# Kernel optimization log

Measured on AMD Instinct MI355X. Metric: run time of the kernel, lower is better.

Reference implementation:

```python
import jax, jax.numpy as jnp
import numpy as np

HIDDEN = 2048
N_HEADS = 32
HEAD_DIM = HIDDEN // N_HEADS
CONV_K = 4
INTER = 5632  # 256*ceil(2048*4*2/3/256)
EPS = 1e-6


def _rms(x, w):
    return x * jax.lax.rsqrt(jnp.mean(x * x, axis=-1, keepdims=True) + EPS) * w


def _l2norm(x):
    n = jnp.sqrt(jnp.sum(x * x, axis=-1, keepdims=True))
    return x / jnp.maximum(n, 1e-12)


def _causal_dwconv(x, w):
    # x [B,T,C], w [C,K] depthwise causal conv (left pad K-1), matches conv1d(pad=K-1)[..., :T]
    C, K = w.shape
    xt = jnp.transpose(x, (0, 2, 1))  # [B,C,T]
    out = jax.lax.conv_general_dilated(
        xt, w[:, None, :], window_strides=(1,), padding=[(K - 1, 0)],
        feature_group_count=C, dimension_numbers=('NCH', 'OIH', 'NCH'))
    return jnp.transpose(out, (0, 2, 1))


def _delta_scan(k, q, v, beta):
    # k,q,v: [B,T,nh,hd]; beta: [B,T,nh]. Per-head state S [hd(v), hd(k)].
    B, T, nh, hd = k.shape
    km, qm, vm = (jnp.moveaxis(a, 1, 0) for a in (k, q, v))  # [T,B,nh,hd]
    bm = jnp.moveaxis(beta, 1, 0)  # [T,B,nh]

    def step(S, inp):
        kt, qt, vt, bt = inp
        err = jnp.einsum('bhvk,bhk->bhv', S, kt) - vt
        S = S - bt[..., None, None] * err[..., None] * kt[..., None, :]
        o = jnp.einsum('bhvk,bhk->bhv', S, qt)
        return S, o

    S0 = jnp.zeros((B, nh, hd, hd), k.dtype)
    S, o = jax.lax.scan(step, S0, (km, qm, vm, bm))
    return jnp.moveaxis(o, 0, 1), S


def setup_inputs() -> dict:
    key = jax.random.key(0)
    ks = jax.random.split(key, 12)
    s = 0.02
    d = {
        'hidden_states': jax.random.normal(ks[0], (1, 1024, HIDDEN), jnp.float32),
        'attn_norm_w': jnp.ones((HIDDEN,), jnp.float32),
        'Wq': jax.random.normal(ks[1], (HIDDEN, HIDDEN), jnp.float32) * s,
        'Wk': jax.random.normal(ks[2], (HIDDEN, HIDDEN), jnp.float32) * s,
        'Wv': jax.random.normal(ks[3], (HIDDEN, HIDDEN), jnp.float32) * s,
        'conv_q': jax.random.normal(ks[4], (HIDDEN, CONV_K), jnp.float32) * 0.1,
        'conv_k': jax.random.normal(ks[5], (HIDDEN, CONV_K), jnp.float32) * 0.1,
        'conv_v': jax.random.normal(ks[6], (HIDDEN, CONV_K), jnp.float32) * 0.1,
        'Wbeta': jax.random.normal(ks[7], (N_HEADS, HIDDEN), jnp.float32) * s,
        'out_norm_w': jnp.ones((HIDDEN,), jnp.float32),
        'Wout': jax.random.normal(ks[8], (HIDDEN, HIDDEN), jnp.float32) * s,
        'mlp_norm_w': jnp.ones((HIDDEN,), jnp.float32),
        'Wgate': jax.random.normal(ks[9], (INTER, HIDDEN), jnp.float32) * s,
        'Wup': jax.random.normal(ks[10], (INTER, HIDDEN), jnp.float32) * s,
        'Wdown': jax.random.normal(ks[11], (HIDDEN, INTER), jnp.float32) * s,
    }
    return d


def reference(hidden_states, attn_norm_w, Wq, Wk, Wv, conv_q, conv_k, conv_v,
              Wbeta, out_norm_w, Wout, mlp_norm_w, Wgate, Wup, Wdown):
    x = hidden_states
    B, T, H = x.shape
    nh, hd = N_HEADS, HEAD_DIM
    silu = jax.nn.silu

    # --- DeltaNet attention sub-block ---
    h = _rms(x, attn_norm_w)
    # proj -> causal depthwise conv -> SiLU (in conv helper) -> SiLU again (forward)
    q = silu(silu(_causal_dwconv(h @ Wq.T, conv_q)))
    k = silu(silu(_causal_dwconv(h @ Wk.T, conv_k)))
    v = silu(silu(_causal_dwconv(h @ Wv.T, conv_v)))
    q = _l2norm(q.reshape(B, T, nh, hd))
    k = _l2norm(k.reshape(B, T, nh, hd))
    v = v.reshape(B, T, nh, hd)
    beta = jax.nn.sigmoid(h @ Wbeta.T)  # [B,T,nh]

    o, memory_state = _delta_scan(k, q, v, beta)
    o = o.reshape(B, T, H)
    o = _rms(o, out_norm_w) @ Wout.T
    x = x + o

    # --- SwiGLU MLP sub-block ---
    h2 = _rms(x, mlp_norm_w)
    gate = h2 @ Wgate.T
    up = h2 @ Wup.T
    x = x + (silu(gate) * up) @ Wdown.T
    return x, memory_state
```

## Files before the change

kernel.cpp:

```cpp
#include <hip/hip_runtime.h>
#include <stdint.h>

typedef unsigned short u16;
typedef unsigned int u32;

#define T_SEQ 1024
#define HID   2048
#define NH    32
#define HD    64
#define NCHUNK 16
#define INTER 5632

typedef __attribute__((ext_vector_type(8))) short b16x8;
typedef __attribute__((ext_vector_type(4))) float f32x4;

__device__ inline float bf2f(u16 u) { union { u32 i; float f; } v; v.i = ((u32)u) << 16; return v.f; }
__device__ inline u16 f2bf(float f) {
  union { float f; u32 i; } v; v.f = f;
  u32 u = v.i;
  return (u16)((u + 0x7FFFu + ((u >> 16) & 1u)) >> 16);
}
__device__ inline float silu_f(float x) { return x / (1.f + __expf(-x)); }

typedef __attribute__((address_space(1))) const unsigned int as1_u32;
typedef __attribute__((address_space(3))) unsigned int as3_u32;
__device__ inline void gl_lds16(const void* g, void* l) {
  __builtin_amdgcn_global_load_lds((as1_u32*)g, (as3_u32*)l, 16, 0, 0);
}

__global__ __launch_bounds__(256) void k_cvt(const float* __restrict__ s, u16* __restrict__ d, int n4) {
  int i = blockIdx.x * 256 + threadIdx.x;
  if (i < n4) {
    float4 v = ((const float4*)s)[i];
    u32 lo = (u32)f2bf(v.x) | ((u32)f2bf(v.y) << 16);
    u32 hi = (u32)f2bf(v.z) | ((u32)f2bf(v.w) << 16);
    ((uint2*)d)[i] = make_uint2(lo, hi);
  }
}

__global__ __launch_bounds__(256) void k_rms(const float* __restrict__ x, const float* __restrict__ w,
                                             u16* __restrict__ out) {
  int row = blockIdx.x, tid = threadIdx.x;
  const float* xr = x + (size_t)row * HID;
  float4 v0 = ((const float4*)xr)[tid];
  float4 v1 = ((const float4*)xr)[tid + 256];
  float ss = v0.x * v0.x + v0.y * v0.y + v0.z * v0.z + v0.w * v0.w +
             v1.x * v1.x + v1.y * v1.y + v1.z * v1.z + v1.w * v1.w;
  for (int m = 32; m; m >>= 1) ss += __shfl_xor(ss, m, 64);
  __shared__ float wsum[4];
  if ((tid & 63) == 0) wsum[tid >> 6] = ss;
  __syncthreads();
  float tot = wsum[0] + wsum[1] + wsum[2] + wsum[3];
  float sc = rsqrtf(tot / (float)HID + 1e-6f);
  float4 w0 = ((const float4*)w)[tid];
  float4 w1 = ((const float4*)w)[tid + 256];
  u32 lo, hi;
  lo = (u32)f2bf(v0.x * sc * w0.x) | ((u32)f2bf(v0.y * sc * w0.y) << 16);
  hi = (u32)f2bf(v0.z * sc * w0.z) | ((u32)f2bf(v0.w * sc * w0.w) << 16);
  ((uint2*)out)[(size_t)row * 512 + tid] = make_uint2(lo, hi);
  lo = (u32)f2bf(v1.x * sc * w1.x) | ((u32)f2bf(v1.y * sc * w1.y) << 16);
  hi = (u32)f2bf(v1.z * sc * w1.z) | ((u32)f2bf(v1.w * sc * w1.w) << 16);
  ((uint2*)out)[(size_t)row * 512 + tid + 256] = make_uint2(lo, hi);
}

__global__ __launch_bounds__(256) void k_gemm(
    const u16* __restrict__ A,
    const u16* __restrict__ B0, const u16* __restrict__ B1, const u16* __restrict__ B2,
    float* __restrict__ C0, float* __restrict__ C1, float* __restrict__ C2,
    const float* __restrict__ resid, int M, int N, int K) {
  const u16* Bp = (blockIdx.z == 0) ? B0 : (blockIdx.z == 1 ? B1 : B2);
  float* Cp = (blockIdx.z == 0) ? C0 : (blockIdx.z == 1 ? C1 : C2);
  __shared__ __align__(16) u16 As[128 * 32];
  __shared__ __align__(16) u16 Bs[128 * 32];
  int tid = threadIdx.x;
  int m0 = blockIdx.y * 128, n0 = blockIdx.x * 128;
  int lane = tid & 63, wv = tid >> 6, wr = wv >> 1, wc = wv & 1;
  int lrow = lane & 15, quad = lane >> 4;
  int lr = lane >> 2, lc = (lane & 3) * 8;
  f32x4 acc[4][4];
#pragma unroll
  for (int i = 0; i < 4; ++i)
#pragma unroll
    for (int j = 0; j < 4; ++j) acc[i][j] = (f32x4){0.f, 0.f, 0.f, 0.f};

  for (int k0 = 0; k0 < K; k0 += 32) {
    const u16* Ag = A + (size_t)(m0 + wv * 32) * K + k0;
    const u16* Bg = Bp + (size_t)(n0 + wv * 32) * K + k0;
    gl_lds16(Ag + (size_t)lr * K + lc,        &As[(wv * 32) * 32]);
    gl_lds16(Ag + (size_t)(16 + lr) * K + lc, &As[(wv * 32 + 16) * 32]);
    gl_lds16(Bg + (size_t)lr * K + lc,        &Bs[(wv * 32) * 32]);
    gl_lds16(Bg + (size_t)(16 + lr) * K + lc, &Bs[(wv * 32 + 16) * 32]);
    __syncthreads();
    b16x8 af[4], bfr[4];
#pragma unroll
    for (int i = 0; i < 4; ++i) af[i] = *(const b16x8*)&As[(wr * 64 + i * 16 + lrow) * 32 + quad * 8];
#pragma unroll
    for (int j = 0; j < 4; ++j) bfr[j] = *(const b16x8*)&Bs[(wc * 64 + j * 16 + lrow) * 32 + quad * 8];
#pragma unroll
    for (int i = 0; i < 4; ++i)
#pragma unroll
      for (int j = 0; j < 4; ++j)
        acc[i][j] = __builtin_amdgcn_mfma_f32_16x16x32_bf16(af[i], bfr[j], acc[i][j], 0, 0, 0);
    __syncthreads();
  }
#pragma unroll
  for (int i = 0; i < 4; ++i)
#pragma unroll
    for (int j = 0; j < 4; ++j)
#pragma unroll
      for (int r = 0; r < 4; ++r) {
        int row = m0 + wr * 64 + i * 16 + quad * 4 + r;
        int col = n0 + wc * 64 + j * 16 + lrow;
        float val = acc[i][j][r];
        if (resid) val += resid[(size_t)row * N + col];
        Cp[(size_t)row * N + col] = val;
      }
}

__global__ __launch_bounds__(256) void k_beta(const u16* __restrict__ hbf, const float* __restrict__ Wb,
                                              float* __restrict__ beta) {
  __shared__ __align__(16) float hr[HID];
  __shared__ float red[256];
  int t = blockIdx.x, tid = threadIdx.x;
#pragma unroll
  for (int i = 0; i < 8; ++i) {
    int c = i * 256 + tid;
    hr[c] = bf2f(hbf[(size_t)t * HID + c]);
  }
  __syncthreads();
  int head = tid >> 3, j = tid & 7;
  const float* wrow = Wb + (size_t)head * HID + j * 256;
  const float* hs = hr + j * 256;
  float acc = 0.f;
#pragma unroll 16
  for (int c = 0; c < 256; c += 4) {
    float4 wv = *(const float4*)&wrow[c];
    float4 hv = *(const float4*)&hs[c];
    acc += hv.x * wv.x + hv.y * wv.y + hv.z * wv.z + hv.w * wv.w;
  }
  red[tid] = acc;
  __syncthreads();
  if (tid < 32) {
    float s = 0.f;
#pragma unroll
    for (int i = 0; i < 8; ++i) s += red[tid * 8 + i];
    beta[(size_t)t * NH + tid] = 1.f / (1.f + __expf(-s));
  }
}

__global__ __launch_bounds__(256) void k_conv(const float* __restrict__ proj,
                                              const float* __restrict__ cw0, const float* __restrict__ cw1,
                                              const float* __restrict__ cw2, float* __restrict__ outp) {
  int z = blockIdx.z;
  const float* src = proj + (size_t)z * T_SEQ * HID;
  float* dst = outp + (size_t)z * T_SEQ * HID;
  const float* cw = (z == 0) ? cw0 : (z == 1 ? cw1 : cw2);
  bool l2 = (z < 2);
  int c = threadIdx.x & 63, wr = threadIdx.x >> 6;
  int head = blockIdx.y;
  int ch = head * 64 + c;
  int t0 = blockIdx.x * 64 + wr * 16;
  float4 w = ((const float4*)cw)[ch];
  float xm3 = (t0 >= 3) ? src[(size_t)(t0 - 3) * HID + ch] : 0.f;
  float xm2 = (t0 >= 2) ? src[(size_t)(t0 - 2) * HID + ch] : 0.f;
  float xm1 = (t0 >= 1) ? src[(size_t)(t0 - 1) * HID + ch] : 0.f;
  for (int i = 0; i < 16; ++i) {
    int t = t0 + i;
    float x0 = src[(size_t)t * HID + ch];
    float zv = xm3 * w.x + xm2 * w.y + xm1 * w.z + x0 * w.w;
    float s = silu_f(silu_f(zv));
    if (l2) {
      float ss = s * s;
      for (int m = 32; m; m >>= 1) ss += __shfl_xor(ss, m, 64);
      float n = sqrtf(ss);
      s = s / fmaxf(n, 1e-12f);
    }
    dst[(size_t)t * HID + ch] = s;
    xm3 = xm2; xm2 = xm1; xm1 = x0;
  }
}

__global__ __launch_bounds__(256) void k_phaseA(
    const float* __restrict__ qp, const float* __restrict__ kp, const float* __restrict__ vp,
    const float* __restrict__ beta,
    u16* __restrict__ negWbf, u16* __restrict__ Uvbf, u16* __restrict__ Ktbf,
    u16* __restrict__ Qbf, u16* __restrict__ Pbf) {
  int cx = blockIdx.x, h = blockIdx.y;
  __shared__ __align__(16) u16 Kst[64 * 72];
  __shared__ __align__(16) u16 Qst[64 * 72];
  __shared__ __align__(16) float Af[64 * 68];
  __shared__ float bet[64];
  int tid = threadIdx.x;
  int t0 = cx * 64;
#pragma unroll
  for (int i = 0; i < 16; ++i) {
    int idx = i * 256 + tid, s = idx >> 6, d = idx & 63;
    size_t g = (size_t)(t0 + s) * HID + h * 64 + d;
    Kst[s * 72 + d] = f2bf(kp[g]);
    Qst[s * 72 + d] = f2bf(qp[g]);
  }
  if (tid < 64) bet[tid] = beta[(size_t)(t0 + tid) * NH + h];
  __syncthreads();
  int lane = tid & 63, wv = tid >> 6, lrow = lane & 15, quad = lane >> 4;
  f32x4 accA[4], accP[4];
#pragma unroll
  for (int i = 0; i < 4; ++i) { accA[i] = (f32x4){0.f, 0.f, 0.f, 0.f}; accP[i] = (f32x4){0.f, 0.f, 0.f, 0.f}; }
#pragma unroll
  for (int ks = 0; ks < 2; ++ks) {
    b16x8 bk = *(const b16x8*)&Kst[(wv * 16 + lrow) * 72 + ks * 32 + quad * 8];
#pragma unroll
    for (int i = 0; i < 4; ++i) {
      b16x8 ak = *(const b16x8*)&Kst[(i * 16 + lrow) * 72 + ks * 32 + quad * 8];
      b16x8 aq = *(const b16x8*)&Qst[(i * 16 + lrow) * 72 + ks * 32 + quad * 8];
      accA[i] = __builtin_amdgcn_mfma_f32_16x16x32_bf16(ak, bk, accA[i], 0, 0, 0);
      accP[i] = __builtin_amdgcn_mfma_f32_16x16x32_bf16(aq, bk, accP[i], 0, 0, 0);
    }
  }
  size_t cb2 = ((size_t)h * NCHUNK + cx) * 4096;
#pragma unroll
  for (int i = 0; i < 4; ++i)
#pragma unroll
    for (int r = 0; r < 4; ++r) {
      int srow = i * 16 + quad * 4 + r, col = wv * 16 + lrow;
      Af[srow * 68 + col] = (col < srow) ? accA[i][r] * bet[srow] : 0.f;
      Pbf[cb2 + srow * 64 + col] = f2bf((col <= srow) ? accP[i][r] : 0.f);
    }
  __syncthreads();
  if (wv < 2) {
    int c = lane;
    float x[64];
    if (wv == 0) {
#pragma unroll
      for (int s = 0; s < 64; ++s) x[s] = bet[s] * bf2f(Kst[s * 72 + c]);
    } else {
#pragma unroll
      for (int s = 0; s < 64; ++s) x[s] = bet[s] * vp[(size_t)(t0 + s) * HID + h * 64 + c];
    }
#pragma unroll
    for (int s = 1; s < 64; ++s) {
      float a = 0.f;
#pragma unroll
      for (int r = 0; r < (s & ~3); r += 4) {
        float4 av = *(const float4*)&Af[s * 68 + r];
        a += av.x * x[r] + av.y * x[r + 1] + av.z * x[r + 2] + av.w * x[r + 3];
      }
#pragma unroll
      for (int r = (s & ~3); r < s; ++r) a += Af[s * 68 + r] * x[r];
      x[s] -= a;
    }
    if (wv == 0) {
#pragma unroll
      for (int s = 0; s < 64; ++s) negWbf[cb2 + s * 64 + c] = f2bf(-x[s]);
    } else {
#pragma unroll
      for (int s = 0; s < 64; ++s) Uvbf[cb2 + s * 64 + c] = f2bf(x[s]);
    }
  } else if (wv == 2) {
#pragma unroll
    for (int it = 0; it < 8; ++it) {
      int cidx = it * 64 + lane, s = cidx >> 3, d0 = (cidx & 7) * 8;
      *(uint4*)&Qbf[cb2 + s * 64 + d0] = *(const uint4*)&Qst[s * 72 + d0];
    }
  } else {
#pragma unroll
    for (int it = 0; it < 8; ++it) {
      int cidx = it * 64 + lane, d = cidx >> 3, s0 = (cidx & 7) * 8;
      u16 tmp[8];
#pragma unroll
      for (int j = 0; j < 8; ++j) tmp[j] = Kst[(s0 + j) * 72 + d];
      *(uint4*)&Ktbf[cb2 + d * 64 + s0] = *(const uint4*)tmp;
    }
  }
}

__global__ __launch_bounds__(256) void k_phaseB1(
    const u16* __restrict__ negWbf, const u16* __restrict__ Uvbf, const u16* __restrict__ Ktbf,
    u16* __restrict__ Utws, u16* __restrict__ Sws, float* __restrict__ Sout) {
  int h = blockIdx.x, tid = threadIdx.x;
  __shared__ __align__(16) u16 S0b[2][64 * 72];
  __shared__ __align__(16) u16 Ut[64 * 72];
  int lane = tid & 63, wv = tid >> 6, lrow = lane & 15, quad = lane >> 4;
#pragma unroll
  for (int i = 0; i < 16; ++i) {
    int idx = i * 256 + tid;
    S0b[0][(idx >> 6) * 72 + (idx & 63)] = 0;
  }
  f32x4 aS[4];
#pragma unroll
  for (int i = 0; i < 4; ++i) aS[i] = (f32x4){0.f, 0.f, 0.f, 0.f};

  b16x8 Wf[2][4][2]; b16x8 Ktf[2][2]; u16 Uvr[2][4][4];
  size_t hb = (size_t)h * NCHUNK * 4096;
  {
    size_t cb2 = hb;
#pragma unroll
    for (int i = 0; i < 4; ++i)
#pragma unroll
      for (int ks = 0; ks < 2; ++ks)
        Wf[0][i][ks] = *(const b16x8*)&negWbf[cb2 + (i * 16 + lrow) * 64 + ks * 32 + quad * 8];
#pragma unroll
    for (int ks = 0; ks < 2; ++ks)
      Ktf[0][ks] = *(const b16x8*)&Ktbf[cb2 + (wv * 16 + lrow) * 64 + ks * 32 + quad * 8];
#pragma unroll
    for (int i = 0; i < 4; ++i)
#pragma unroll
      for (int r = 0; r < 4; ++r)
        Uvr[0][i][r] = Uvbf[cb2 + (i * 16 + quad * 4 + r) * 64 + wv * 16 + lrow];
  }
  __syncthreads();
#pragma unroll
  for (int cx = 0; cx < NCHUNK; ++cx) {
    const int p = cx & 1, q = p ^ 1;
    size_t cb2 = hb + (size_t)cx * 4096;
    if (cx > 0) {
#pragma unroll
      for (int i = 0; i < 2; ++i) {
        int cidx = i * 256 + tid, dv = cidx >> 3, s0 = (cidx & 7) * 8;
        *(uint4*)&Sws[cb2 + dv * 64 + s0] = *(const uint4*)&S0b[p][dv * 72 + s0];
      }
    }
    if (cx + 1 < NCHUNK) {
      size_t cbn = cb2 + 4096;
#pragma unroll
      for (int i = 0; i < 4; ++i)
#pragma unroll
        for (int ks = 0; ks < 2; ++ks)
          Wf[q][i][ks] = *(const b16x8*)&negWbf[cbn + (i * 16 + lrow) * 64 + ks * 32 + quad * 8];
#pragma unroll
      for (int ks = 0; ks < 2; ++ks)
        Ktf[q][ks] = *(const b16x8*)&Ktbf[cbn + (wv * 16 + lrow) * 64 + ks * 32 + quad * 8];
#pragma unroll
      for (int i = 0; i < 4; ++i)
#pragma unroll
        for (int r = 0; r < 4; ++r)
          Uvr[q][i][r] = Uvbf[cbn + (i * 16 + quad * 4 + r) * 64 + wv * 16 + lrow];
    }
    f32x4 aU[4];
#pragma unroll
    for (int i = 0; i < 4; ++i)
#pragma unroll
      for (int r = 0; r < 4; ++r) aU[i][r] = bf2f(Uvr[p][i][r]);
#pragma unroll
    for (int ks = 0; ks < 2; ++ks) {
      b16x8 bS = *(const b16x8*)&S0b[p][(wv * 16 + lrow) * 72 + ks * 32 + quad * 8];
#pragma unroll
      for (int i = 0; i < 4; ++i)
        aU[i] = __builtin_amdgcn_mfma_f32_16x16x32_bf16(Wf[p][i][ks], bS, aU[i], 0, 0, 0);
    }
#pragma unroll
    for (int i = 0; i < 4; ++i)
#pragma unroll
      for (int r = 0; r < 4; ++r) {
        int s = i * 16 + quad * 4 + r, dv = wv * 16 + lrow;
        Ut[dv * 72 + s] = f2bf(aU[i][r]);
      }
    __syncthreads();
#pragma unroll
    for (int i = 0; i < 2; ++i) {
      int cidx = i * 256 + tid, dv = cidx >> 3, s0 = (cidx & 7) * 8;
      *(uint4*)&Utws[cb2 + dv * 64 + s0] = *(const uint4*)&Ut[dv * 72 + s0];
    }
#pragma unroll
    for (int ks = 0; ks < 2; ++ks) {
#pragma unroll
      for (int i = 0; i < 4; ++i) {
        b16x8 a = *(const b16x8*)&Ut[(i * 16 + lrow) * 72 + ks * 32 + quad * 8];
        aS[i] = __builtin_amdgcn_mfma_f32_16x16x32_bf16(a, Ktf[p][ks], aS[i], 0, 0, 0);
      }
    }
#pragma unroll
    for (int i = 0; i < 4; ++i)
#pragma unroll
      for (int r = 0; r < 4; ++r) {
        int dv = i * 16 + quad * 4 + r, dk = wv * 16 + lrow;
        S0b[q][dv * 72 + dk] = f2bf(aS[i][r]);
      }
    __syncthreads();
  }
#pragma unroll
  for (int i = 0; i < 4; ++i)
#pragma unroll
    for (int r = 0; r < 4; ++r) {
      int dv = i * 16 + quad * 4 + r, dk = wv * 16 + lrow;
      Sout[(size_t)h * 4096 + dv * 64 + dk] = aS[i][r];
    }
}

__global__ __launch_bounds__(256) void k_phaseB2(
    const u16* __restrict__ Qbf, const u16* __restrict__ Pbf,
    const u16* __restrict__ Utws, const u16* __restrict__ Sws, float* __restrict__ o) {
  int cx = blockIdx.x, h = blockIdx.y, tid = threadIdx.x;
  int lane = tid & 63, wv = tid >> 6, lrow = lane & 15, quad = lane >> 4;
  size_t cb2 = ((size_t)h * NCHUNK + cx) * 4096;
  f32x4 aO[4];
#pragma unroll
  for (int i = 0; i < 4; ++i) aO[i] = (f32x4){0.f, 0.f, 0.f, 0.f};
#pragma unroll
  for (int ks = 0; ks < 2; ++ks) {
    b16x8 Uf = *(const b16x8*)&Utws[cb2 + (wv * 16 + lrow) * 64 + ks * 32 + quad * 8];
#pragma unroll
    for (int i = 0; i < 4; ++i) {
      b16x8 Pf = *(const b16x8*)&Pbf[cb2 + (i * 16 + lrow) * 64 + ks * 32 + quad * 8];
      aO[i] = __builtin_amdgcn_mfma_f32_16x16x32_bf16(Pf, Uf, aO[i], 0, 0, 0);
    }
  }
  if (cx > 0) {
#pragma unroll
    for (int ks = 0; ks < 2; ++ks) {
      b16x8 Sf = *(const b16x8*)&Sws[cb2 + (wv * 16 + lrow) * 64 + ks * 32 + quad * 8];
#pragma unroll
      for (int i = 0; i < 4; ++i) {
        b16x8 Qf = *(const b16x8*)&Qbf[cb2 + (i * 16 + lrow) * 64 + ks * 32 + quad * 8];
        aO[i] = __builtin_amdgcn_mfma_f32_16x16x32_bf16(Qf, Sf, aO[i], 0, 0, 0);
      }
    }
  }
  int t0 = cx * 64;
#pragma unroll
  for (int i = 0; i < 4; ++i)
#pragma unroll
    for (int r = 0; r < 4; ++r)
      o[(size_t)(t0 + i * 16 + quad * 4 + r) * HID + h * 64 + wv * 16 + lrow] = aO[i][r];
}

__global__ __launch_bounds__(256) void k_swiglu(const float* __restrict__ g, const float* __restrict__ u,
                                                u16* __restrict__ d) {
  int i = blockIdx.x * 256 + threadIdx.x;
  float4 gv = ((const float4*)g)[i];
  float4 uv = ((const float4*)u)[i];
  u32 lo = (u32)f2bf(silu_f(gv.x) * uv.x) | ((u32)f2bf(silu_f(gv.y) * uv.y) << 16);
  u32 hi = (u32)f2bf(silu_f(gv.z) * uv.z) | ((u32)f2bf(silu_f(gv.w) * uv.w) << 16);
  ((uint2*)d)[i] = make_uint2(lo, hi);
}

extern "C" void kernel_launch(void* const* d_in, const int* in_sizes, int n_in,
                              void* d_out, int out_size, void* d_ws, size_t ws_size,
                              hipStream_t stream) {
  const float* x     = (const float*)d_in[0];
  const float* anw   = (const float*)d_in[1];
  const float* Wq    = (const float*)d_in[2];
  const float* Wk    = (const float*)d_in[3];
  const float* Wv    = (const float*)d_in[4];
  const float* convq = (const float*)d_in[5];
  const float* convk = (const float*)d_in[6];
  const float* convv = (const float*)d_in[7];
  const float* Wbeta = (const float*)d_in[8];
  const float* onw   = (const float*)d_in[9];
  const float* Wout  = (const float*)d_in[10];
  const float* mnw   = (const float*)d_in[11];
  const float* Wgate = (const float*)d_in[12];
  const float* Wup   = (const float*)d_in[13];
  const float* Wdown = (const float*)d_in[14];
  float* out = (float*)d_out;

  const size_t TH = (size_t)T_SEQ * HID;
  const size_t SCAN = (size_t)NH * NCHUNK * 4096;
  char* wsb = (char*)d_ws;
  size_t off = 0;
  auto alloc = [&](size_t bytes) -> void* {
    void* p = wsb + off;
    off += (bytes + 255) & ~(size_t)255;
    return p;
  };
  u16* wq_bf    = (u16*)alloc((size_t)HID * HID * 2);
  u16* wk_bf    = (u16*)alloc((size_t)HID * HID * 2);
  u16* wv_bf    = (u16*)alloc((size_t)HID * HID * 2);
  u16* wout_bf  = (u16*)alloc((size_t)HID * HID * 2);
  u16* wgate_bf = (u16*)alloc((size_t)INTER * HID * 2);
  u16* wup_bf   = (u16*)alloc((size_t)INTER * HID * 2);
  u16* wdown_bf = (u16*)alloc((size_t)HID * INTER * 2);
  u16* actbf    = (u16*)alloc(TH * 2);
  float* qkv_proj = (float*)alloc(3 * TH * 4);
  float* qkvpost  = (float*)alloc(3 * TH * 4);
  float* betab    = (float*)alloc((size_t)T_SEQ * NH * 4);
  u16* negWbf = (u16*)alloc(SCAN * 2);
  u16* Uvbf   = (u16*)alloc(SCAN * 2);
  u16* Ktbf   = (u16*)alloc(SCAN * 2);
  u16* Qbf    = (u16*)alloc(SCAN * 2);
  u16* Pbf    = (u16*)alloc(SCAN * 2);
  u16* Utws   = (u16*)alloc(SCAN * 2);
  u16* Sws    = (u16*)alloc(SCAN * 2);
  float* x1   = (float*)alloc(TH * 4);
  float* obuf = qkv_proj;
  float* gate = qkv_proj;
  float* up   = qkvpost;
  u16* g_bf   = negWbf;

  auto cvt = [&](const float* s, u16* d, size_t n) {
    int n4 = (int)(n / 4);
    k_cvt<<<dim3((n4 + 255) / 256), 256, 0, stream>>>(s, d, n4);
  };
  cvt(Wq, wq_bf, (size_t)HID * HID);
  cvt(Wk, wk_bf, (size_t)HID * HID);
  cvt(Wv, wv_bf, (size_t)HID * HID);
  cvt(Wout, wout_bf, (size_t)HID * HID);
  cvt(Wgate, wgate_bf, (size_t)INTER * HID);
  cvt(Wup, wup_bf, (size_t)INTER * HID);
  cvt(Wdown, wdown_bf, (size_t)HID * INTER);

  k_rms<<<dim3(T_SEQ), 256, 0, stream>>>(x, anw, actbf);
  k_gemm<<<dim3(HID / 128, T_SEQ / 128, 3), 256, 0, stream>>>(
      actbf, wq_bf, wk_bf, wv_bf, qkv_proj, qkv_proj + TH, qkv_proj + 2 * TH, nullptr,
      T_SEQ, HID, HID);
  k_beta<<<dim3(T_SEQ), 256, 0, stream>>>(actbf, Wbeta, betab);
  k_conv<<<dim3(T_SEQ / 64, NH, 3), 256, 0, stream>>>(qkv_proj, convq, convk, convv, qkvpost);
  k_phaseA<<<dim3(NCHUNK, NH), 256, 0, stream>>>(
      qkvpost, qkvpost + TH, qkvpost + 2 * TH, betab, negWbf, Uvbf, Ktbf, Qbf, Pbf);
  k_phaseB1<<<dim3(NH), 256, 0, stream>>>(negWbf, Uvbf, Ktbf, Utws, Sws, out + TH);
  k_phaseB2<<<dim3(NCHUNK, NH), 256, 0, stream>>>(Qbf, Pbf, Utws, Sws, obuf);
  k_rms<<<dim3(T_SEQ), 256, 0, stream>>>(obuf, onw, actbf);
  k_gemm<<<dim3(HID / 128, T_SEQ / 128, 1), 256, 0, stream>>>(
      actbf, wout_bf, wout_bf, wout_bf, x1, x1, x1, x, T_SEQ, HID, HID);
  k_rms<<<dim3(T_SEQ), 256, 0, stream>>>(x1, mnw, actbf);
  k_gemm<<<dim3(INTER / 128, T_SEQ / 128, 2), 256, 0, stream>>>(
      actbf, wgate_bf, wup_bf, wup_bf, gate, up, up, nullptr, T_SEQ, INTER, HID);
  k_swiglu<<<dim3((T_SEQ * INTER / 4) / 256), 256, 0, stream>>>(gate, up, g_bf);
  k_gemm<<<dim3(HID / 128, T_SEQ / 128, 1), 256, 0, stream>>>(
      g_bf, wdown_bf, wdown_bf, wdown_bf, out, out, out, x1, T_SEQ, HID, INTER);
}
```

Before: 709.0 us.

## Add split-K GEMMs, fuse gate/up with SwiGLU, swizzle LDS, batch weight conversion

The separate weight-conversion launches are merged into one 2D-grid kernel. The GEMM gains a split-K mode that accumulates with atomicAdd into zeroed outputs, giving more blocks on the smaller 1024x2048 GEMMs. Its LDS reads use an XOR swizzle to cut bank conflicts. The gate and up projections now run in a single kernel that applies SiLU*up in its epilogue and writes bf16 directly, which removes the fp32 gate/up round trip and the separate swiglu launch. In exchange the code adds memsets, atomic traffic and non-deterministic summation order, and the fused gate/up kernel holds two accumulator sets, which raises register pressure.

```diff
diff --git a/kernel.cpp b/kernel.cpp
--- a/kernel.cpp
+++ b/kernel.cpp
@@ -28,14 +28,24 @@
   __builtin_amdgcn_global_load_lds((as1_u32*)g, (as3_u32*)l, 16, 0, 0);
 }
 
-__global__ __launch_bounds__(256) void k_cvt(const float* __restrict__ s, u16* __restrict__ d, int n4) {
+__global__ __launch_bounds__(256) void k_cvt_all(
+    const float* __restrict__ s0, const float* __restrict__ s1, const float* __restrict__ s2,
+    const float* __restrict__ s3, const float* __restrict__ s4, const float* __restrict__ s5,
+    const float* __restrict__ s6,
+    u16* __restrict__ d0, u16* __restrict__ d1, u16* __restrict__ d2, u16* __restrict__ d3,
+    u16* __restrict__ d4, u16* __restrict__ d5, u16* __restrict__ d6) {
+  int z = blockIdx.y;
+  int n4 = (z < 4) ? (HID * HID / 4) : (INTER * HID / 4);
   int i = blockIdx.x * 256 + threadIdx.x;
-  if (i < n4) {
-    float4 v = ((const float4*)s)[i];
-    u32 lo = (u32)f2bf(v.x) | ((u32)f2bf(v.y) << 16);
-    u32 hi = (u32)f2bf(v.z) | ((u32)f2bf(v.w) << 16);
-    ((uint2*)d)[i] = make_uint2(lo, hi);
-  }
+  if (i >= n4) return;
+  const float* s = (z == 0) ? s0 : (z == 1) ? s1 : (z == 2) ? s2 : (z == 3) ? s3
+                   : (z == 4) ? s4 : (z == 5) ? s5 : s6;
+  u16* d = (z == 0) ? d0 : (z == 1) ? d1 : (z == 2) ? d2 : (z == 3) ? d3
+           : (z == 4) ? d4 : (z == 5) ? d5 : d6;
+  float4 v = ((const float4*)s)[i];
+  u32 lo = (u32)f2bf(v.x) | ((u32)f2bf(v.y) << 16);
+  u32 hi = (u32)f2bf(v.z) | ((u32)f2bf(v.w) << 16);
+  ((uint2*)d)[i] = make_uint2(lo, hi);
 }
 
 __global__ __launch_bounds__(256) void k_rms(const float* __restrict__ x, const float* __restrict__ w,
@@ -63,39 +73,43 @@
   ((uint2*)out)[(size_t)row * 512 + tid + 256] = make_uint2(lo, hi);
 }
 
-__global__ __launch_bounds__(256) void k_gemm(
+__global__ __launch_bounds__(256) void k_gemm_sk(
     const u16* __restrict__ A,
     const u16* __restrict__ B0, const u16* __restrict__ B1, const u16* __restrict__ B2,
     float* __restrict__ C0, float* __restrict__ C1, float* __restrict__ C2,
-    const float* __restrict__ resid, int M, int N, int K) {
-  const u16* Bp = (blockIdx.z == 0) ? B0 : (blockIdx.z == 1 ? B1 : B2);
-  float* Cp = (blockIdx.z == 0) ? C0 : (blockIdx.z == 1 ? C1 : C2);
+    const float* __restrict__ resid, int M, int N, int Kf, int KS, int nslice) {
+  int mat = blockIdx.z / nslice, slice = blockIdx.z % nslice;
+  const u16* Bp = (mat == 0) ? B0 : (mat == 1 ? B1 : B2);
+  float* Cp = (mat == 0) ? C0 : (mat == 1 ? C1 : C2);
   __shared__ __align__(16) u16 As[128 * 32];
   __shared__ __align__(16) u16 Bs[128 * 32];
   int tid = threadIdx.x;
   int m0 = blockIdx.y * 128, n0 = blockIdx.x * 128;
   int lane = tid & 63, wv = tid >> 6, wr = wv >> 1, wc = wv & 1;
   int lrow = lane & 15, quad = lane >> 4;
-  int lr = lane >> 2, lc = (lane & 3) * 8;
+  int lr = lane >> 2;
+  int lc = (((lane & 3) ^ ((lr >> 1) & 3)) * 8);
+  int xq = quad ^ ((lrow >> 1) & 3);
   f32x4 acc[4][4];
 #pragma unroll
   for (int i = 0; i < 4; ++i)
 #pragma unroll
     for (int j = 0; j < 4; ++j) acc[i][j] = (f32x4){0.f, 0.f, 0.f, 0.f};
 
-  for (int k0 = 0; k0 < K; k0 += 32) {
-    const u16* Ag = A + (size_t)(m0 + wv * 32) * K + k0;
-    const u16* Bg = Bp + (size_t)(n0 + wv * 32) * K + k0;
-    gl_lds16(Ag + (size_t)lr * K + lc,        &As[(wv * 32) * 32]);
-    gl_lds16(Ag + (size_t)(16 + lr) * K + lc, &As[(wv * 32 + 16) * 32]);
-    gl_lds16(Bg + (size_t)lr * K + lc,        &Bs[(wv * 32) * 32]);
-    gl_lds16(Bg + (size_t)(16 + lr) * K + lc, &Bs[(wv * 32 + 16) * 32]);
+  int kb = slice * KS, ke = kb + KS;
+  for (int k0 = kb; k0 < ke; k0 += 32) {
+    const u16* Ag = A + (size_t)(m0 + wv * 32) * Kf + k0;
+    const u16* Bg = Bp + (size_t)(n0 + wv * 32) * Kf + k0;
+    gl_lds16(Ag + (size_t)lr * Kf + lc,        &As[(wv * 32) * 32]);
+    gl_lds16(Ag + (size_t)(16 + lr) * Kf + lc, &As[(wv * 32 + 16) * 32]);
+    gl_lds16(Bg + (size_t)lr * Kf + lc,        &Bs[(wv * 32) * 32]);
+    gl_lds16(Bg + (size_t)(16 + lr) * Kf + lc, &Bs[(wv * 32 + 16) * 32]);
     __syncthreads();
     b16x8 af[4], bfr[4];
 #pragma unroll
-    for (int i = 0; i < 4; ++i) af[i] = *(const b16x8*)&As[(wr * 64 + i * 16 + lrow) * 32 + quad * 8];
-#pragma unroll
-    for (int j = 0; j < 4; ++j) bfr[j] = *(const b16x8*)&Bs[(wc * 64 + j * 16 + lrow) * 32 + quad * 8];
+    for (int i = 0; i < 4; ++i) af[i] = *(const b16x8*)&As[(wr * 64 + i * 16 + lrow) * 32 + xq * 8];
+#pragma unroll
+    for (int j = 0; j < 4; ++j) bfr[j] = *(const b16x8*)&Bs[(wc * 64 + j * 16 + lrow) * 32 + xq * 8];
 #pragma unroll
     for (int i = 0; i < 4; ++i)
 #pragma unroll
@@ -112,8 +126,66 @@
         int row = m0 + wr * 64 + i * 16 + quad * 4 + r;
         int col = n0 + wc * 64 + j * 16 + lrow;
         float val = acc[i][j][r];
-        if (resid) val += resid[(size_t)row * N + col];
-        Cp[(size_t)row * N + col] = val;
+        if (slice == 0 && resid) val += resid[(size_t)row * N + col];
+        atomicAdd(&Cp[(size_t)row * N + col], val);
+      }
+}
+
+__global__ __launch_bounds__(256) void k_gemm_gu(
+    const u16* __restrict__ A, const u16* __restrict__ Bg, const u16* __restrict__ Bu,
+    u16* __restrict__ D) {
+  __shared__ __align__(16) u16 As[128 * 32];
+  __shared__ __align__(16) u16 Gs[128 * 32];
+  __shared__ __align__(16) u16 Us[128 * 32];
+  int tid = threadIdx.x;
+  int m0 = blockIdx.y * 128, n0 = blockIdx.x * 128;
+  int lane = tid & 63, wv = tid >> 6, wr = wv >> 1, wc = wv & 1;
+  int lrow = lane & 15, quad = lane >> 4;
+  int lr = lane >> 2;
+  int lc = (((lane & 3) ^ ((lr >> 1) & 3)) * 8);
+  int xq = quad ^ ((lrow >> 1) & 3);
+  f32x4 ag[4][4], au[4][4];
+#pragma unroll
+  for (int i = 0; i < 4; ++i)
+#pragma unroll
+    for (int j = 0; j < 4; ++j) { ag[i][j] = (f32x4){0.f, 0.f, 0.f, 0.f}; au[i][j] = (f32x4){0.f, 0.f, 0.f, 0.f}; }
+
+  for (int k0 = 0; k0 < HID; k0 += 32) {
+    const u16* Ap = A + (size_t)(m0 + wv * 32) * HID + k0;
+    const u16* Gp = Bg + (size_t)(n0 + wv * 32) * HID + k0;
+    const u16* Up = Bu + (size_t)(n0 + wv * 32) * HID + k0;
+    gl_lds16(Ap + (size_t)lr * HID + lc,        &As[(wv * 32) * 32]);
+    gl_lds16(Ap + (size_t)(16 + lr) * HID + lc, &As[(wv * 32 + 16) * 32]);
+    gl_lds16(Gp + (size_t)lr * HID + lc,        &Gs[(wv * 32) * 32]);
+    gl_lds16(Gp + (size_t)(16 + lr) * HID + lc, &Gs[(wv * 32 + 16) * 32]);
+    gl_lds16(Up + (size_t)lr * HID + lc,        &Us[(wv * 32) * 32]);
+    gl_lds16(Up + (size_t)(16 + lr) * HID + lc, &Us[(wv * 32 + 16) * 32]);
+    __syncthreads();
+    b16x8 af[4], gf[4], uf[4];
+#pragma unroll
+    for (int i = 0; i < 4; ++i) af[i] = *(const b16x8*)&As[(wr * 64 + i * 16 + lrow) * 32 + xq * 8];
+#pragma unroll
+    for (int j = 0; j < 4; ++j) gf[j] = *(const b16x8*)&Gs[(wc * 64 + j * 16 + lrow) * 32 + xq * 8];
+#pragma unroll
+    for (int j = 0; j < 4; ++j) uf[j] = *(const b16x8*)&Us[(wc * 64 + j * 16 + lrow) * 32 + xq * 8];
+#pragma unroll
+    for (int i = 0; i < 4; ++i)
+#pragma unroll
+      for (int j = 0; j < 4; ++j) {
+        ag[i][j] = __builtin_amdgcn_mfma_f32_16x16x32_bf16(af[i], gf[j], ag[i][j], 0, 0, 0);
+        au[i][j] = __builtin_amdgcn_mfma_f32_16x16x32_bf16(af[i], uf[j], au[i][j], 0, 0, 0);
+      }
+    __syncthreads();
+  }
+#pragma unroll
+  for (int i = 0; i < 4; ++i)
+#pragma unroll
+    for (int j = 0; j < 4; ++j)
+#pragma unroll
+      for (int r = 0; r < 4; ++r) {
+        int row = m0 + wr * 64 + i * 16 + quad * 4 + r;
+        int col = n0 + wc * 64 + j * 16 + lrow;
+        D[(size_t)row * INTER + col] = f2bf(silu_f(ag[i][j][r]) * au[i][j][r]);
       }
 }
 
@@ -421,16 +493,6 @@
 #pragma unroll
     for (int r = 0; r < 4; ++r)
       o[(size_t)(t0 + i * 16 + quad * 4 + r) * HID + h * 64 + wv * 16 + lrow] = aO[i][r];
-}
-
-__global__ __launch_bounds__(256) void k_swiglu(const float* __restrict__ g, const float* __restrict__ u,
-                                                u16* __restrict__ d) {
-  int i = blockIdx.x * 256 + threadIdx.x;
-  float4 gv = ((const float4*)g)[i];
-  float4 uv = ((const float4*)u)[i];
-  u32 lo = (u32)f2bf(silu_f(gv.x) * uv.x) | ((u32)f2bf(silu_f(gv.y) * uv.y) << 16);
-  u32 hi = (u32)f2bf(silu_f(gv.z) * uv.z) | ((u32)f2bf(silu_f(gv.w) * uv.w) << 16);
-  ((uint2*)d)[i] = make_uint2(lo, hi);
 }
 
 extern "C" void kernel_launch(void* const* d_in, const int* in_sizes, int n_in,
@@ -482,26 +544,17 @@
   u16* Sws    = (u16*)alloc(SCAN * 2);
   float* x1   = (float*)alloc(TH * 4);
   float* obuf = qkv_proj;
-  float* gate = qkv_proj;
-  float* up   = qkvpost;
   u16* g_bf   = negWbf;
 
-  auto cvt = [&](const float* s, u16* d, size_t n) {
-    int n4 = (int)(n / 4);
-    k_cvt<<<dim3((n4 + 255) / 256), 256, 0, stream>>>(s, d, n4);
-  };
-  cvt(Wq, wq_bf, (size_t)HID * HID);
-  cvt(Wk, wk_bf, (size_t)HID * HID);
-  cvt(Wv, wv_bf, (size_t)HID * HID);
-  cvt(Wout, wout_bf, (size_t)HID * HID);
-  cvt(Wgate, wgate_bf, (size_t)INTER * HID);
-  cvt(Wup, wup_bf, (size_t)INTER * HID);
-  cvt(Wdown, wdown_bf, (size_t)HID * INTER);
+  k_cvt_all<<<dim3(INTER * HID / 4 / 256, 7), 256, 0, stream>>>(
+      Wq, Wk, Wv, Wout, Wgate, Wup, Wdown,
+      wq_bf, wk_bf, wv_bf, wout_bf, wgate_bf, wup_bf, wdown_bf);
 
   k_rms<<<dim3(T_SEQ), 256, 0, stream>>>(x, anw, actbf);
-  k_gemm<<<dim3(HID / 128, T_SEQ / 128, 3), 256, 0, stream>>>(
+  hipMemsetAsync(qkv_proj, 0, 3 * TH * 4, stream);
+  k_gemm_sk<<<dim3(HID / 128, T_SEQ / 128, 6), 256, 0, stream>>>(
       actbf, wq_bf, wk_bf, wv_bf, qkv_proj, qkv_proj + TH, qkv_proj + 2 * TH, nullptr,
-      T_SEQ, HID, HID);
+      T_SEQ, HID, HID, HID / 2, 2);
   k_beta<<<dim3(T_SEQ), 256, 0, stream>>>(actbf, Wbeta, betab);
   k_conv<<<dim3(T_SEQ / 64, NH, 3), 256, 0, stream>>>(qkv_proj, convq, convk, convv, qkvpost);
   k_phaseA<<<dim3(NCHUNK, NH), 256, 0, stream>>>(
@@ -509,12 +562,12 @@
   k_phaseB1<<<dim3(NH), 256, 0, stream>>>(negWbf, Uvbf, Ktbf, Utws, Sws, out + TH);
   k_phaseB2<<<dim3(NCHUNK, NH), 256, 0, stream>>>(Qbf, Pbf, Utws, Sws, obuf);
   k_rms<<<dim3(T_SEQ), 256, 0, stream>>>(obuf, onw, actbf);
-  k_gemm<<<dim3(HID / 128, T_SEQ / 128, 1), 256, 0, stream>>>(
-      actbf, wout_bf, wout_bf, wout_bf, x1, x1, x1, x, T_SEQ, HID, HID);
+  hipMemsetAsync(x1, 0, TH * 4, stream);
+  k_gemm_sk<<<dim3(HID / 128, T_SEQ / 128, 4), 256, 0, stream>>>(
+      actbf, wout_bf, wout_bf, wout_bf, x1, x1, x1, x, T_SEQ, HID, HID, HID / 4, 4);
   k_rms<<<dim3(T_SEQ), 256, 0, stream>>>(x1, mnw, actbf);
-  k_gemm<<<dim3(INTER / 128, T_SEQ / 128, 2), 256, 0, stream>>>(
-      actbf, wgate_bf, wup_bf, wup_bf, gate, up, up, nullptr, T_SEQ, INTER, HID);
-  k_swiglu<<<dim3((T_SEQ * INTER / 4) / 256), 256, 0, stream>>>(gate, up, g_bf);
-  k_gemm<<<dim3(HID / 128, T_SEQ / 128, 1), 256, 0, stream>>>(
-      g_bf, wdown_bf, wdown_bf, wdown_bf, out, out, out, x1, T_SEQ, HID, INTER);
-}
+  k_gemm_gu<<<dim3(INTER / 128, T_SEQ / 128), 256, 0, stream>>>(actbf, wgate_bf, wup_bf, g_bf);
+  hipMemsetAsync(out, 0, TH * 4, stream);
+  k_gemm_sk<<<dim3(HID / 128, T_SEQ / 128, 4), 256, 0, stream>>>(
+      g_bf, wdown_bf, wdown_bf, wdown_bf, out, out, out, x1, T_SEQ, HID, INTER, INTER / 4, 4);
+}
```

Measured after the change: 706.3 us. No clear change (-0.4%).
